# Kernel tuning notes

Measured on AMD Instinct MI355X. Metric: run time of the kernel, lower is better.

## Reference

```python
import jax, jax.numpy as jnp
import numpy as np

B, S, D = 2, 2048, 2048
H, DN, DR, DV = 16, 128, 64, 128   # heads, qk_nope, qk_rope, v_head
Q_LORA, KV_LORA = 1536, 512
DQ = DN + DR                        # qk_head_dim = 192
EPS = 1e-6


def setup_inputs() -> dict:
    key = jax.random.key(0)
    ks = jax.random.split(key, 8)
    s = 0.02  # weight init scale
    hidden_states = jax.random.normal(ks[0], (B, S, D), jnp.float32)
    # RoPE tables (non-interleaved HF style: cat(freqs, freqs)) per position
    inv_freq = 1.0 / (10000.0 ** (np.arange(0, DR, 2, dtype=np.float32) / DR))
    freqs = np.arange(S, dtype=np.float32)[:, None] * inv_freq[None, :]  # [S, DR/2]
    emb = np.concatenate([freqs, freqs], axis=-1)                        # [S, DR]
    cos = jnp.broadcast_to(jnp.asarray(np.cos(emb)), (B, S, DR))
    sin = jnp.broadcast_to(jnp.asarray(np.sin(emb)), (B, S, DR))
    return {
        'hidden_states': hidden_states,
        'cos': cos, 'sin': sin,
        'Wqa': jax.random.normal(ks[1], (D, Q_LORA), jnp.float32) * s,
        'qa_ln_w': jnp.ones((Q_LORA,), jnp.float32),
        'Wqb': jax.random.normal(ks[2], (Q_LORA, H * DQ), jnp.float32) * s,
        'Wkva': jax.random.normal(ks[3], (D, KV_LORA + DR), jnp.float32) * s,
        'kva_ln_w': jnp.ones((KV_LORA,), jnp.float32),
        'Wkvb': jax.random.normal(ks[4], (KV_LORA, H * (DN + DV)), jnp.float32) * s,
        'Wo': jax.random.normal(ks[5], (H * DV, D), jnp.float32) * s,
    }


def _rmsnorm(x, w):
    xf = x.astype(jnp.float32)
    var = jnp.mean(xf * xf, axis=-1, keepdims=True)
    return w * (xf * jax.lax.rsqrt(var + EPS)).astype(x.dtype)


def _rotate_half(x):
    h = x.shape[-1] // 2
    return jnp.concatenate([-x[..., h:], x[..., :h]], axis=-1)


def reference(hidden_states, cos, sin, Wqa, qa_ln_w, Wqb, Wkva, kva_ln_w, Wkvb, Wo):
    b, s, _ = hidden_states.shape
    scaling = DQ ** -0.5

    # Q path: down-proj -> RMSNorm -> up-proj -> [b, H, s, DQ]
    q = _rmsnorm(hidden_states @ Wqa, qa_ln_w) @ Wqb
    q = q.reshape(b, s, H, DQ).transpose(0, 2, 1, 3)
    q_pass, q_rot = q[..., :DN], q[..., DN:]

    # KV path: joint down-proj -> split latent / shared rope key
    ckv = hidden_states @ Wkva                       # [b, s, KV_LORA + DR]
    k_lat, k_rot = ckv[..., :KV_LORA], ckv[..., KV_LORA:]
    kv = _rmsnorm(k_lat, kva_ln_w) @ Wkvb            # [b, s, H*(DN+DV)]
    kv = kv.reshape(b, s, H, DN + DV).transpose(0, 2, 1, 3)
    k_pass, v = kv[..., :DN], kv[..., DN:]

    # decoupled RoPE on q_rot and the single shared k_rot head
    k_rot = k_rot[:, None, :, :]                     # [b, 1, s, DR]
    c, si = cos[:, None], sin[:, None]               # unsqueeze_dim=1
    q_rot = q_rot * c + _rotate_half(q_rot) * si
    k_rot = k_rot * c + _rotate_half(k_rot) * si
    k_rot = jnp.broadcast_to(k_rot, (b, H, s, DR))

    Q = jnp.concatenate([q_pass, q_rot], axis=-1)    # [b, H, s, DQ]
    K = jnp.concatenate([k_pass, k_rot], axis=-1)

    scores = jnp.einsum('bhqd,bhkd->bhqk', Q, K) * scaling
    neg = jnp.finfo(jnp.float32).min
    causal = jnp.where(jnp.tril(jnp.ones((s, s), bool)), 0.0, neg)
    scores = scores + causal
    w = jax.nn.softmax(scores.astype(jnp.float32), axis=-1).astype(Q.dtype)

    out = jnp.einsum('bhqk,bhkd->bhqd', w, v)
    out = out.transpose(0, 2, 1, 3).reshape(b, s, H * DV)
    return out @ Wo
```

## Files before the change

### kernel.cpp

```cpp
#include <hip/hip_runtime.h>
#include <math.h>

#define BB 2
#define SS 2048
#define DD 2048
#define HH 16
#define DN 128
#define DR 64
#define DV 128
#define QL 1536
#define KVL 512
#define DQ 192
#define CKVS 640
#define KVD 256
#define NCAT 2176
#define NCATP 2304
#define EPSF 1e-6f

typedef short bfrag __attribute__((ext_vector_type(8)));
typedef float facc  __attribute__((ext_vector_type(4)));

__device__ __forceinline__ ushort f2bf(float f) {
    union { float f; unsigned u; } v; v.f = f;
    unsigned r = v.u + 0x7fffu + ((v.u >> 16) & 1u);
    return (ushort)(r >> 16);
}
__device__ __forceinline__ float bf2f(ushort u) {
    union { unsigned u; float f; } v; v.u = ((unsigned)u) << 16;
    return v.f;
}
__device__ __forceinline__ float fexp2(float x) {
    float r; asm("v_exp_f32 %0, %1" : "=v"(r) : "v"(x)); return r;
}
__device__ __forceinline__ float wave_red_sum(float v) {
    #pragma unroll
    for (int o = 32; o > 0; o >>= 1) v += __shfl_down(v, o);
    return v;
}
__device__ __forceinline__ void gl2lds16(const ushort* g, ushort* l) {
    __builtin_amdgcn_global_load_lds(
        (const __attribute__((address_space(1))) void*)g,
        (__attribute__((address_space(3))) void*)l, 16, 0, 0);
}

__global__ __launch_bounds__(256) void castf2bf(const float* __restrict__ x,
                                                ushort* __restrict__ y) {
    const int i = blockIdx.x * 256 + threadIdx.x;
    const float4 v = ((const float4*)x)[i];
    ushort4 o;
    o.x = f2bf(v.x); o.y = f2bf(v.y); o.z = f2bf(v.z); o.w = f2bf(v.w);
    ((ushort4*)y)[i] = o;
}

struct WtBatch {
    const float* src[2];
    ushort* dst[2];
    int K[2];
    int N[2];
    int nx[2];
    int base[3];
};
__global__ __launch_bounds__(256) void wtrans_b(WtBatch d) {
    __shared__ float tile[32][33];
    int bid = blockIdx.x;
    int seg = (bid >= d.base[1]) ? 1 : 0;
    const int l = bid - d.base[seg];
    const int nx = d.nx[seg];
    const int bx = l % nx, by = l / nx;
    const float* W = d.src[seg];
    ushort* Wt = d.dst[seg];
    const int K = d.K[seg], N = d.N[seg];
    const int k0 = by * 32, n0 = bx * 32;
    const int t = threadIdx.x;
    const int tx = t & 31, ty = t >> 5;
    #pragma unroll
    for (int r = 0; r < 4; ++r) {
        const int n = n0 + tx;
        tile[ty + r * 8][tx] =
            (n < N) ? W[(size_t)(k0 + ty + r * 8) * N + n] : 0.f;
    }
    __syncthreads();
    #pragma unroll
    for (int r = 0; r < 4; ++r) {
        const int n = n0 + ty + r * 8;
        Wt[(size_t)n * K + k0 + tx] = f2bf(tile[tx][ty + r * 8]);
    }
}


__device__ __forceinline__ void stage_half(const ushort* __restrict__ G,
                                           int ldg, int grow0, int kcol0,
                                           ushort* Lr, int wave, int lane) {
    const int r0   = lane >> 3;
    const int slot = (lane & 7) ^ r0;
    const ushort* s0 = G + (size_t)(grow0 + wave * 16 + r0) * ldg + kcol0 + slot * 8;
    gl2lds16(s0,                    Lr + wave * 1024);
    gl2lds16(s0 + (size_t)8 * ldg,  Lr + wave * 1024 + 512);
}

#define PH_PRE  do { __builtin_amdgcn_sched_barrier(0);                      \
                     __builtin_amdgcn_s_barrier();                           \
                     asm volatile("s_waitcnt lgkmcnt(0)" ::: "memory");      \
                     __builtin_amdgcn_sched_barrier(0);                      \
                     __builtin_amdgcn_s_setprio(1); } while (0)
#define PH_POST do { __builtin_amdgcn_s_setprio(0);                          \
                     __builtin_amdgcn_sched_barrier(0);                      \
                     __builtin_amdgcn_s_barrier(); } while (0)

#define MFMA16(RB)                                                           \
    _Pragma("unroll")                                                        \
    for (int i = 0; i < 4; ++i)                                              \
        _Pragma("unroll")                                                    \
        for (int j = 0; j < 4; ++j)                                          \
            acc[(RB) + i][j] = __builtin_amdgcn_mfma_f32_16x16x32_bf16(      \
                a[i], b[j], acc[(RB) + i][j], 0, 0, 0);

#define GEMM256_CORE(A_, Bt_, K_, NBX_, LID_)                                 \
    const int t    = threadIdx.x;                                             \
    const int lane = t & 63;                                                  \
    const int wave = t >> 6;                                                  \
    const int wm   = wave >> 2;                                               \
    const int wn   = wave & 3;                                                \
    const int quad = lane >> 4;                                               \
    const int lrow = lane & 15;                                               \
    const int bx = (LID_) % (NBX_), by = (LID_) / (NBX_);                     \
    const int m0 = by * 256, n0 = bx * 256;                                   \
    const int s0x8  = (quad ^ (lrow & 7)) * 8;       \
    const int s1x8  = s0x8 ^ 32;                   \
    const int abase = lrow * 64;                                              \
    const int bbase = (wn & 1) * 4096 + lrow * 64;                            \
    facc acc[8][4];                                                           \
    _Pragma("unroll")                                                         \
    for (int i = 0; i < 8; ++i)                                               \
        _Pragma("unroll")                                                     \
        for (int j = 0; j < 4; ++j) acc[i][j] = (facc)(0.f);                  \
    const int nk = (K_) >> 6;                                                 \
    stage_half((A_),  (K_), m0,        0, L,         wave, lane);             \
    stage_half((A_),  (K_), m0 + 128,  0, L + 8192,  wave, lane);             \
    stage_half((Bt_), (K_), n0,        0, L + 16384, wave, lane);             \
    stage_half((Bt_), (K_), n0 + 128,  0, L + 24576, wave, lane);             \
    stage_half((Bt_), (K_), n0,       64, L + 49152, wave, lane);             \
    stage_half((Bt_), (K_), n0 + 128, 64, L + 57344, wave, lane);             \
    asm volatile("s_waitcnt vmcnt(4)" ::: "memory");                          \
    __builtin_amdgcn_s_barrier();                                             \
    for (int kt = 0; kt < nk; ++kt) {                                         \
        const int p = kt & 1;                                                 \
        ushort* LA = L + p * 32768 + wm * 8192;                               \
        ushort* LB = L + p * 32768 + 16384 + (wn >> 1) * 8192;                \
        ushort* Lq = L + (p ^ 1) * 32768;                                     \
        const int kn = (kt + 1) * 64;                                         \
        bfrag a[4], b[4];                                                     \
        _Pragma("unroll")                                                     \
        for (int i = 0; i < 4; ++i)                                           \
            a[i] = *(const bfrag*)(LA + i * 1024 + abase + s0x8);             \
        _Pragma("unroll")                                                     \
        for (int j = 0; j < 4; ++j)                                           \
            b[j] = *(const bfrag*)(LB + bbase + j * 1024 + s0x8);             \
        if (kt + 1 < nk) stage_half((A_), (K_), m0, kn, Lq, wave, lane);      \
        PH_PRE;                                                               \
        MFMA16(0)                                                             \
        PH_POST;                                                              \
        _Pragma("unroll")                                                     \
        for (int i = 0; i < 4; ++i)                                           \
            a[i] = *(const bfrag*)(LA + (4 + i) * 1024 + abase + s0x8);       \
        if (kt + 1 < nk)                                                      \
            stage_half((A_), (K_), m0 + 128, kn, Lq + 8192, wave, lane);      \
        PH_PRE;                                                               \
        MFMA16(4)                                                             \
        PH_POST;                                                              \
        _Pragma("unroll")                                                     \
        for (int i = 0; i < 4; ++i)                                           \
            a[i] = *(const bfrag*)(LA + i * 1024 + abase + s1x8);             \
        _Pragma("unroll")                                                     \
        for (int j = 0; j < 4; ++j)                                           \
            b[j] = *(const bfrag*)(LB + bbase + j * 1024 + s1x8);             \
        PH_PRE;                                                               \
        MFMA16(0)                                                             \
        PH_POST;                                                              \
        _Pragma("unroll")                                                     \
        for (int i = 0; i < 4; ++i)                                           \
            a[i] = *(const bfrag*)(LA + (4 + i) * 1024 + abase + s1x8);       \
        if (kt + 2 < nk) {                                                    \
            stage_half((Bt_), (K_), n0,       kn + 64,                        \
                       L + p * 32768 + 16384, wave, lane);                    \
            stage_half((Bt_), (K_), n0 + 128, kn + 64,                        \
                       L + p * 32768 + 24576, wave, lane);                    \
            asm volatile("s_waitcnt vmcnt(4)" ::: "memory");                  \
        } else {                                                              \
            asm volatile("s_waitcnt vmcnt(0)" ::: "memory");                  \
        }                                                                     \
        PH_PRE;                                                               \
        MFMA16(4)                                                             \
        PH_POST;                                                              \
    }

#define GEMMW_CORE(A_, Bt_, K_, NBX_, LID_)                                   \
    const int t    = threadIdx.x;                                             \
    const int lane = t & 63;                                                  \
    const int wave = t >> 6;                                                  \
    const int wm   = wave >> 1;                                     \
    const int wn   = wave & 1;                                      \
    const int quad = lane >> 4;                                               \
    const int lrow = lane & 15;                                               \
    const int bx = (LID_) % (NBX_), by = (LID_) / (NBX_);                     \
    const int m0 = by * 256, n0 = bx * 128;                                   \
    const int s0x8 = (quad ^ (lrow & 7)) * 8;                                 \
    const int s1x8 = s0x8 ^ 32;                                               \
    facc acc[4][4];                                                           \
    _Pragma("unroll")                                                         \
    for (int i = 0; i < 4; ++i)                                               \
        _Pragma("unroll")                                                     \
        for (int j = 0; j < 4; ++j) acc[i][j] = (facc)(0.f);                  \
    const int nk = (K_) >> 6;                                                 \
    stage_half((A_),  (K_), m0,        0, L,          wave, lane);            \
    stage_half((A_),  (K_), m0 + 128,  0, L + 8192,   wave, lane);            \
    stage_half((Bt_), (K_), n0,        0, L + 32768,  wave, lane);            \
    stage_half((Bt_), (K_), n0,       64, L + 40960,  wave, lane);            \
    asm volatile("s_waitcnt vmcnt(0)" ::: "memory");                          \
    __builtin_amdgcn_s_barrier();                                             \
    int bp = 0, bp2 = 2;                               \
    for (int kt = 0; kt < nk; ++kt) {                                         \
        const int p = kt & 1;                                                 \
        ushort* LA = L + p * 16384 + (wm >> 1) * 8192                         \
                       + ((wm & 1) * 64 + lrow) * 64;                         \
        ushort* LB = L + 32768 + bp * 8192 + (wn * 64 + lrow) * 64;           \
        const int kn = (kt + 1) * 64;                                         \
        bfrag a[4], b[4];                                                     \
        _Pragma("unroll")                                                     \
        for (int i = 0; i < 4; ++i) a[i] = *(const bfrag*)(LA + i * 1024 + s0x8); \
        _Pragma("unroll")                                                     \
        for (int j = 0; j < 4; ++j) b[j] = *(const bfrag*)(LB + j * 1024 + s0x8); \
        if (kt + 1 < nk) {                                                    \
            stage_half((A_), (K_), m0,       kn, L + (p ^ 1) * 16384,        wave, lane); \
            stage_half((A_), (K_), m0 + 128, kn, L + (p ^ 1) * 16384 + 8192, wave, lane); \
        }                                                                     \
        if (kt + 2 < nk)                                                      \
            stage_half((Bt_), (K_), n0, kn + 64, L + 32768 + bp2 * 8192, wave, lane); \
        PH_PRE;                                                               \
        MFMA16(0)                                                             \
        PH_POST;                                                              \
        _Pragma("unroll")                                                     \
        for (int i = 0; i < 4; ++i) a[i] = *(const bfrag*)(LA + i * 1024 + s1x8); \
        _Pragma("unroll")                                                     \
        for (int j = 0; j < 4; ++j) b[j] = *(const bfrag*)(LB + j * 1024 + s1x8); \
        if (kt + 2 < nk) { asm volatile("s_waitcnt vmcnt(2)" ::: "memory"); } \
        else             { asm volatile("s_waitcnt vmcnt(0)" ::: "memory"); } \
        PH_PRE;                                                               \
        MFMA16(0)                                                             \
        PH_POST;                                                              \
        bp  = (bp  == 2) ? 0 : bp  + 1;                                       \
        bp2 = (bp2 == 2) ? 0 : bp2 + 1;                                       \
    }

template <int K, int NBX, int NOUT>
__global__ __launch_bounds__(512, 2) void gemmW(const ushort* __restrict__ A,
                                                const ushort* __restrict__ Bt,
                                                float* __restrict__ C) {
    __shared__ ushort L[57344];
    int wg = (int)blockIdx.x;
    { const int cpx = (int)gridDim.x >> 3; wg = (wg & 7) * cpx + (wg >> 3); }
    GEMMW_CORE(A, Bt, K, NBX, wg)
    #pragma unroll
    for (int m = 0; m < 4; ++m) {
        const int row = m0 + wm * 64 + m * 16 + quad * 4;
        #pragma unroll
        for (int nf = 0; nf < 4; ++nf) {
            const int col = n0 + wn * 64 + nf * 16 + lrow;
            #pragma unroll
            for (int r = 0; r < 4; ++r)
                C[(size_t)(row + r) * NOUT + col] = acc[m][nf][r];
        }
    }
}

__global__ __launch_bounds__(512, 2) void gemmAW(
    const ushort* __restrict__ A,   const ushort* __restrict__ Bt,
    ushort* __restrict__ qa,        ushort* __restrict__ ckv,
    const float* __restrict__ Wqb,  ushort* __restrict__ Wqbt,
    const float* __restrict__ Wkvb, ushort* __restrict__ Wkvbt,
    const float* __restrict__ Wo,   ushort* __restrict__ Wot) {
    __shared__ ushort L[65536];
    const int bid = (int)blockIdx.x;
    if (bid < 144) {
        const int lid = (bid & 7) * 18 + (bid >> 3);
        GEMM256_CORE(A, Bt, DD, 9, lid)
        #pragma unroll
        for (int m = 0; m < 8; ++m) {
            const int row = m0 + wm * 128 + m * 16 + quad * 4;
            #pragma unroll
            for (int nf = 0; nf < 4; ++nf) {
                const int col = n0 + wn * 64 + nf * 16 + lrow;
                #pragma unroll
                for (int r = 0; r < 4; ++r) {
                    if (col < QL)
                        qa[(size_t)(row + r) * QL + col] = f2bf(acc[m][nf][r]);
                    else if (col < NCAT)
                        ckv[(size_t)(row + r) * CKVS + col - QL] = f2bf(acc[m][nf][r]);
                }
            }
        }
    } else {
        const int wid = bid - 144;
        const int t   = threadIdx.x;
        const int half = t >> 8;
        const int tl = t & 255;
        const int tx = tl & 31, ty = tl >> 5;
        float (*tile)[33] = (float(*)[33])((float*)L + half * 32 * 33);
        for (int it = 0; it < 48; ++it) {
            const int idx = (it * 112 + wid) * 2 + half;
            const float* W; ushort* Wt; int K, N, nx, l;
            if (idx < 4608)      { l = idx;        W = Wqb;  Wt = Wqbt;  K = QL;  N = HH * DQ;  nx = 96; }
            else if (idx < 6656) { l = idx - 4608; W = Wkvb; Wt = Wkvbt; K = KVL; N = HH * KVD; nx = 128; }
            else                 { l = idx - 6656; W = Wo;   Wt = Wot;   K = DD;  N = DD;       nx = 64; }
            const int bx2 = l % nx, by2 = l / nx;
            const int k0 = by2 * 32, n0w = bx2 * 32;
            #pragma unroll
            for (int r = 0; r < 4; ++r)
                tile[ty + r * 8][tx] = W[(size_t)(k0 + ty + r * 8) * N + n0w + tx];
            __syncthreads();
            #pragma unroll
            for (int r = 0; r < 4; ++r)
                Wt[(size_t)(n0w + ty + r * 8) * K + k0 + tx] = f2bf(tile[tx][ty + r * 8]);
            __syncthreads();
        }
    }
}

__global__ __launch_bounds__(512, 2) void gemmQKV(
    const ushort* __restrict__ qa,  const ushort* __restrict__ Wqbt,
    ushort* __restrict__ Qbuf,
    const ushort* __restrict__ kvn, const ushort* __restrict__ Wkvbt,
    ushort* __restrict__ kvb) {
    __shared__ ushort L[65536];
    const int bid = (int)blockIdx.x;
    if (bid < 192) {
        const int lid = (bid & 7) * 24 + (bid >> 3);
        GEMM256_CORE(qa, Wqbt, QL, 12, lid)
        const float scaling = 0.10411754831f;
        #pragma unroll
        for (int m = 0; m < 8; ++m) {
            const int row = m0 + wm * 128 + m * 16 + quad * 4;
            #pragma unroll
            for (int nf = 0; nf < 4; ++nf) {
                const int col = n0 + wn * 64 + nf * 16 + lrow;
                const int h = col / DQ, d = col - h * DQ;
                #pragma unroll
                for (int r = 0; r < 4; ++r) {
                    const int tok = row + r;
                    const int b = tok >> 11, s2 = tok & (SS - 1);
                    Qbuf[((size_t)(b * HH + h) * SS + s2) * DQ + d] =
                        f2bf(acc[m][nf][r] * scaling);
                }
            }
        }
    } else {
        const int b2 = bid - 192;
        const int lid = (b2 & 7) * 32 + (b2 >> 3);
        GEMM256_CORE(kvn, Wkvbt, KVL, 16, lid)
        #pragma unroll
        for (int m = 0; m < 8; ++m) {
            const int row = m0 + wm * 128 + m * 16 + quad * 4;
            #pragma unroll
            for (int nf = 0; nf < 4; ++nf) {
                const int col = n0 + wn * 64 + nf * 16 + lrow;
                #pragma unroll
                for (int r = 0; r < 4; ++r)
                    kvb[(size_t)(row + r) * (HH * KVD) + col] = f2bf(acc[m][nf][r]);
            }
        }
    }
}

__global__ __launch_bounds__(256) void rmsnorm2(ushort* __restrict__ qa,
                                                const float* __restrict__ qaw,
                                                const ushort* __restrict__ ckv,
                                                const float* __restrict__ kvw,
                                                ushort* __restrict__ kvn,
                                                ushort* __restrict__ krb,
                                                const float* __restrict__ cosb,
                                                const float* __restrict__ sinb) {
    __shared__ float red[4];
    const int t = threadIdx.x;
    const int lane = t & 63, wid = t >> 6;
    const int bid = (int)blockIdx.x;
    if (bid < BB * SS) {
        ushort* xr = qa + (size_t)bid * QL;
        float ss = 0.f;
        for (int i = t; i < QL; i += 256) { float v = bf2f(xr[i]); ss += v * v; }
        ss = wave_red_sum(ss);
        if (lane == 0) red[wid] = ss;
        __syncthreads();
        const float tot = red[0] + red[1] + red[2] + red[3];
        const float sc = rsqrtf(tot / (float)QL + EPSF);
        for (int i = t; i < QL; i += 256) xr[i] = f2bf(qaw[i] * bf2f(xr[i]) * sc);
    } else {
        const int row = bid - BB * SS;
        const ushort* xr = ckv + (size_t)row * CKVS;
        ushort* yr = kvn + (size_t)row * KVL;
        if (t < 64) {
            const int p = t;
            const ushort* kin = xr + KVL;
            const float c  = cosb[(size_t)row * DR + p];
            const float sn = sinb[(size_t)row * DR + p];
            const float self = bf2f(kin[p]);
            const float partner = bf2f(kin[p < 32 ? p + 32 : p - 32]);
            const float v = (p < 32) ? (self * c - partner * sn)
                                     : (self * c + partner * sn);
            krb[(size_t)row * DR + p] = f2bf(v);
        }
        float ss = 0.f;
        for (int i = t; i < KVL; i += 256) { float v = bf2f(xr[i]); ss += v * v; }
        ss = wave_red_sum(ss);
        if (lane == 0) red[wid] = ss;
        __syncthreads();
        const float tot = red[0] + red[1] + red[2] + red[3];
        const float sc = rsqrtf(tot / (float)KVL + EPSF);
        for (int i = t; i < KVL; i += 256) yr[i] = f2bf(kvw[i] * bf2f(xr[i]) * sc);
    }
}

__global__ __launch_bounds__(256) void ropevprep(ushort* __restrict__ Qbuf,
                                                 const float* __restrict__ cosb,
                                                 const float* __restrict__ sinb,
                                                 const ushort* __restrict__ kvb,
                                                 ushort* __restrict__ Vtb) {
    __shared__ ushort tile[32][33];
    const int bid = (int)blockIdx.x;
    const int t = threadIdx.x;
    if (bid < BB * SS) {
        const int tok = bid;
        const int b = tok >> 11, s = tok & (SS - 1);
        const int p = t & 31, hh = t >> 5;
        const float c0 = cosb[(size_t)tok * DR + p];
        const float s0 = sinb[(size_t)tok * DR + p];
        const float c1 = cosb[(size_t)tok * DR + p + 32];
        const float s1 = sinb[(size_t)tok * DR + p + 32];
        #pragma unroll
        for (int it = 0; it < 2; ++it) {
            const int h = hh + it * 8;
            ushort* base = Qbuf + ((size_t)(b * HH + h) * SS + s) * DQ + DN;
            const float x0 = bf2f(base[p]), x1 = bf2f(base[p + 32]);
            base[p]      = f2bf(x0 * c0 - x1 * s0);
            base[p + 32] = f2bf(x1 * c1 + x0 * s1);
        }
    } else {
        const int v = bid - BB * SS;
        const int kp0 = (v & 63) * 32;
        const int dv0 = ((v >> 6) & 3) * 32;
        const int bh  = v >> 8;
        const int b = bh / HH, h = bh - b * HH;
        const int tx = t & 31, ty = t >> 5;
        #pragma unroll
        for (int r = 0; r < 4; ++r)
            tile[ty + r * 8][tx] =
                kvb[(size_t)(b * SS + kp0 + ty + r * 8) * (HH * KVD) + h * KVD + DN + dv0 + tx];
        __syncthreads();
        #pragma unroll
        for (int r = 0; r < 4; ++r)
            Vtb[((size_t)bh * DV + dv0 + ty + r * 8) * SS + kp0 + tx] = tile[tx][ty + r * 8];
    }
}

__global__ __launch_bounds__(256, 2) void fattn_mfma(
    const ushort* __restrict__ Qb,
    const ushort* __restrict__ kvb,
    const ushort* __restrict__ krb,
    const ushort* __restrict__ Vt,
    ushort* __restrict__ o)
{
    const int h  = blockIdx.y;
    const int b  = blockIdx.z;
    const int qt = b ? (15 - (int)blockIdx.x) : (int)blockIdx.x;
    const int bh = b * HH + h;
    const int q0 = qt * 128;
    const int t    = threadIdx.x;
    const int lane = t & 63;
    const int wave = t >> 6;
    const int quad = lane >> 4;
    const int n    = lane & 15;
    const int wstrip = wave * 16;

    __shared__ ushort Ksu[6 * 64 * 32];
    __shared__ ushort Vtu[2 * 128 * 32];
    __shared__ ushort Psu[2 * 128 * 40];

    const ushort* vbase = Vt + (size_t)bh * DV * SS;

    bfrag aQ[2][6];
    #pragma unroll
    for (int sp = 0; sp < 2; ++sp) {
        const ushort* qrow = Qb + ((size_t)bh * SS + q0 + sp * 64 + wstrip + n) * DQ;
        #pragma unroll
        for (int kb = 0; kb < 6; ++kb)
            aQ[sp][kb] = *(const bfrag*)(qrow + kb * 32 + quad * 8);
    }

    facc oacc[2][8];
    float lp[2][4];
    #pragma unroll
    for (int sp = 0; sp < 2; ++sp) {
        #pragma unroll
        for (int jd = 0; jd < 8; ++jd) oacc[sp][jd] = (facc)(0.f);
        #pragma unroll
        for (int r = 0; r < 4; ++r) lp[sp][r] = 0.f;
    }

    #pragma unroll
    for (int i = 0; i < 6; ++i) {
        const int g = wave + 4 * i;
        const int kb = g >> 2;
        const int rem = (g & 3) * 64 + lane;
        const int row = rem >> 2, sub = rem & 3;
        const int tok = b * SS + row;
        const ushort* src = (kb < 4)
            ? kvb + (size_t)tok * (HH * KVD) + h * KVD + kb * 32 + sub * 8
            : krb + (size_t)tok * DR + (kb - 4) * 32 + sub * 8;
        gl2lds16(src, Ksu + g * 512);
    }
    #pragma unroll
    for (int i = 0; i < 4; ++i) {
        const int g = wave + 4 * i;
        const int kb2 = g >> 3;
        const int rem = (g & 7) * 64 + lane;
        const int dv = rem >> 2, sub = rem & 3;
        gl2lds16(vbase + (size_t)dv * SS + kb2 * 32 + sub * 8, Vtu + g * 512);
    }
    __syncthreads();

    const int nkt = 2 * qt + 2;
    for (int kt = 0; kt < nkt; ++kt) {
        const int k0 = kt * 64;
        const int kk = (kt + 1 < nkt) ? (k0 + 64) : (SS - 64);

        bfrag kreg[6], vreg[4];
        #pragma unroll
        for (int i = 0; i < 6; ++i) {
            const int g = wave + 4 * i;
            const int kb = g >> 2;
            const int rem = (g & 3) * 64 + lane;
            const int row = rem >> 2, sub = rem & 3;
            const int tok = b * SS + kk + row;
            const ushort* src = (kb < 4)
                ? kvb + (size_t)tok * (HH * KVD) + h * KVD + kb * 32 + sub * 8
                : krb + (size_t)tok * DR + (kb - 4) * 32 + sub * 8;
            kreg[i] = *(const bfrag*)src;
        }
        #pragma unroll
        for (int i = 0; i < 4; ++i) {
            const int g = wave + 4 * i;
            const int kb2 = g >> 3;
            const int rem = (g & 7) * 64 + lane;
            const int dv = rem >> 2, sub = rem & 3;
            vreg[i] = *(const bfrag*)(vbase + (size_t)dv * SS + kk + kb2 * 32 + sub * 8);
        }
        __builtin_amdgcn_sched_barrier(0);

        facc s[2][4];
        #pragma unroll
        for (int sp = 0; sp < 2; ++sp)
            #pragma unroll
            for (int j = 0; j < 4; ++j) s[sp][j] = (facc)(0.f);
        #pragma unroll
        for (int kb = 0; kb < 6; ++kb) {
            #pragma unroll
            for (int j = 0; j < 4; ++j) {
                const bfrag bk =
                    *(const bfrag*)&Ksu[kb * 2048 + (j * 16 + n) * 32 + quad * 8];
                s[0][j] = __builtin_amdgcn_mfma_f32_16x16x32_bf16(aQ[0][kb], bk, s[0][j], 0, 0, 0);
                s[1][j] = __builtin_amdgcn_mfma_f32_16x16x32_bf16(aQ[1][kb], bk, s[1][j], 0, 0, 0);
            }
        }

        const bool fullt = (k0 + 64 <= q0);
        if (fullt) {
            #pragma unroll
            for (int sp = 0; sp < 2; ++sp) {
                #pragma unroll
                for (int j = 0; j < 4; ++j) {
                    #pragma unroll
                    for (int r = 0; r < 4; ++r) {
                        const float p = fexp2(s[sp][j][r]);
                        lp[sp][r] += p;
                        Psu[(j >> 1) * 5120 + (sp * 64 + wstrip + quad * 4 + r) * 40
                            + (j & 1) * 16 + n] = f2bf(p);
                    }
                }
            }
        } else {
            #pragma unroll
            for (int sp = 0; sp < 2; ++sp) {
                const int rowg0 = q0 + sp * 64 + wstrip + quad * 4;
                #pragma unroll
                for (int j = 0; j < 4; ++j) {
                    const int kpos = k0 + j * 16 + n;
                    #pragma unroll
                    for (int r = 0; r < 4; ++r) {
                        const float p = (kpos <= rowg0 + r) ? fexp2(s[sp][j][r]) : 0.f;
                        lp[sp][r] += p;
                        Psu[(j >> 1) * 5120 + (sp * 64 + wstrip + quad * 4 + r) * 40
                            + (j & 1) * 16 + n] = f2bf(p);
                    }
                }
            }
        }

        #pragma unroll
        for (int kb2 = 0; kb2 < 2; ++kb2) {
            const bfrag aP0 = *(const bfrag*)&Psu[kb2 * 5120 + (wstrip + n) * 40 + quad * 8];
            const bfrag aP1 = *(const bfrag*)&Psu[kb2 * 5120 + (64 + wstrip + n) * 40 + quad * 8];
            #pragma unroll
            for (int jd = 0; jd < 8; ++jd) {
                const bfrag bV = *(const bfrag*)&Vtu[kb2 * 4096 + (jd * 16 + n) * 32 + quad * 8];
                oacc[0][jd] = __builtin_amdgcn_mfma_f32_16x16x32_bf16(aP0, bV, oacc[0][jd], 0, 0, 0);
                oacc[1][jd] = __builtin_amdgcn_mfma_f32_16x16x32_bf16(aP1, bV, oacc[1][jd], 0, 0, 0);
            }
        }

        __syncthreads();
        #pragma unroll
        for (int i = 0; i < 6; ++i)
            *(bfrag*)(Ksu + (wave + 4 * i) * 512 + lane * 8) = kreg[i];
        #pragma unroll
        for (int i = 0; i < 4; ++i)
            *(bfrag*)(Vtu + (wave + 4 * i) * 512 + lane * 8) = vreg[i];
        __syncthreads();
    }

    #pragma unroll
    for (int sp = 0; sp < 2; ++sp) {
        #pragma unroll
        for (int r = 0; r < 4; ++r) {
            float v = lp[sp][r];
            #pragma unroll
            for (int msk = 1; msk < 16; msk <<= 1) v += __shfl_xor(v, msk);
            const float inv = 1.f / v;
            ushort* op = o + (size_t)(b * SS + q0 + sp * 64 + wstrip + quad * 4 + r)
                             * (HH * DV) + h * DV;
            #pragma unroll
            for (int jd = 0; jd < 8; ++jd)
                op[jd * 16 + n] = f2bf(oacc[sp][jd][r] * inv);
        }
    }
}

extern "C" void kernel_launch(void* const* d_in, const int* in_sizes, int n_in,
                              void* d_out, int out_size, void* d_ws, size_t ws_size,
                              hipStream_t stream) {
    const float* hs    = (const float*)d_in[0];
    const float* cosb  = (const float*)d_in[1];
    const float* sinb  = (const float*)d_in[2];
    const float* Wqa   = (const float*)d_in[3];
    const float* qa_w  = (const float*)d_in[4];
    const float* Wqb   = (const float*)d_in[5];
    const float* Wkva  = (const float*)d_in[6];
    const float* kva_w = (const float*)d_in[7];
    const float* Wkvb  = (const float*)d_in[8];
    const float* Wo    = (const float*)d_in[9];
    float* out = (float*)d_out;

    const int T = BB * SS;

    char* w = (char*)d_ws;
    auto alloc = [&](size_t bytes) {
        void* r = (void*)w;
        w += (bytes + 255) & ~(size_t)255;
        return r;
    };
    ushort* hs_bf  = (ushort*)alloc((size_t)T * DD * 2);
    ushort* Wcat   = (ushort*)alloc((size_t)NCATP * DD * 2);
    ushort* Wqbt   = (ushort*)alloc((size_t)(HH * DQ) * QL * 2);
    ushort* Wkvbt  = (ushort*)alloc((size_t)(HH * KVD) * KVL * 2);
    ushort* Wot    = (ushort*)alloc((size_t)DD * DD * 2);
    ushort* qa_bf  = (ushort*)alloc((size_t)T * QL * 2);
    ushort* Qbuf   = (ushort*)alloc((size_t)T * HH * DQ * 2);
    ushort* ckv_bf = (ushort*)alloc((size_t)T * CKVS * 2);
    ushort* kvn_bf = (ushort*)alloc((size_t)T * KVL * 2);
    ushort* kv_bf  = (ushort*)alloc((size_t)T * HH * KVD * 2);
    ushort* krb    = (ushort*)alloc((size_t)T * DR * 2);
    ushort* Vtb    = Wcat;
    ushort* ao_bf  = hs_bf;

    castf2bf<<<(T * DD / 4) / 256, 256, 0, stream>>>(hs, hs_bf);
    WtBatch wb;
    wb.src[0] = Wqa;  wb.dst[0] = Wcat;                   wb.K[0] = DD; wb.N[0] = QL;       wb.nx[0] = 48;
    wb.src[1] = Wkva; wb.dst[1] = Wcat + (size_t)QL * DD; wb.K[1] = DD; wb.N[1] = KVL + DR; wb.nx[1] = 20;
    wb.base[0] = 0;
    wb.base[1] = wb.nx[0] * (DD / 32);
    wb.base[2] = wb.base[1] + wb.nx[1] * (DD / 32);
    wtrans_b<<<wb.base[2], 256, 0, stream>>>(wb);

    gemmAW<<<dim3(256), 512, 0, stream>>>(hs_bf, Wcat, qa_bf, ckv_bf,
                                          Wqb, Wqbt, Wkvb, Wkvbt, Wo, Wot);
    rmsnorm2<<<2 * T, 256, 0, stream>>>(qa_bf, qa_w, ckv_bf, kva_w, kvn_bf,
                                        krb, cosb, sinb);
    gemmQKV<<<dim3(448), 512, 0, stream>>>(qa_bf, Wqbt, Qbuf,
                                           kvn_bf, Wkvbt, kv_bf);
    ropevprep<<<T + 8192, 256, 0, stream>>>(Qbuf, cosb, sinb, kv_bf, Vtb);
    fattn_mfma<<<dim3(16, HH, BB), 256, 0, stream>>>(Qbuf, kv_bf, krb, Vtb, ao_bf);
    gemmW<DD, 16, DD><<<dim3(256), 512, 0, stream>>>(ao_bf, Wot, out);
}
```

Measured before the change: 403.0 us.

## Split attention strips across 8 waves and use 256x256 tiles for output GEMM

The flash-attention kernel now runs with 512 threads per block, so each wave handles one 16-row query strip instead of two. This halves per-wave registers and raises the occupancy bound to 4. The output projection drops the 256x128-tile gemmW and uses the existing 256x256 GEMM256 core with 128 blocks, which gives more reuse per tile. The risk is fewer blocks for the output GEMM, plus fewer MFMAs per LDS load and more LDS contention in attention.

```diff
diff --git a/kernel.cpp b/kernel.cpp
--- a/kernel.cpp
+++ b/kernel.cpp
@@ -194,81 +194,22 @@
         PH_POST;                                                              \
     }
 
-#define GEMMW_CORE(A_, Bt_, K_, NBX_, LID_)                                   \
-    const int t    = threadIdx.x;                                             \
-    const int lane = t & 63;                                                  \
-    const int wave = t >> 6;                                                  \
-    const int wm   = wave >> 1;                                     \
-    const int wn   = wave & 1;                                      \
-    const int quad = lane >> 4;                                               \
-    const int lrow = lane & 15;                                               \
-    const int bx = (LID_) % (NBX_), by = (LID_) / (NBX_);                     \
-    const int m0 = by * 256, n0 = bx * 128;                                   \
-    const int s0x8 = (quad ^ (lrow & 7)) * 8;                                 \
-    const int s1x8 = s0x8 ^ 32;                                               \
-    facc acc[4][4];                                                           \
-    _Pragma("unroll")                                                         \
-    for (int i = 0; i < 4; ++i)                                               \
-        _Pragma("unroll")                                                     \
-        for (int j = 0; j < 4; ++j) acc[i][j] = (facc)(0.f);                  \
-    const int nk = (K_) >> 6;                                                 \
-    stage_half((A_),  (K_), m0,        0, L,          wave, lane);            \
-    stage_half((A_),  (K_), m0 + 128,  0, L + 8192,   wave, lane);            \
-    stage_half((Bt_), (K_), n0,        0, L + 32768,  wave, lane);            \
-    stage_half((Bt_), (K_), n0,       64, L + 40960,  wave, lane);            \
-    asm volatile("s_waitcnt vmcnt(0)" ::: "memory");                          \
-    __builtin_amdgcn_s_barrier();                                             \
-    int bp = 0, bp2 = 2;                               \
-    for (int kt = 0; kt < nk; ++kt) {                                         \
-        const int p = kt & 1;                                                 \
-        ushort* LA = L + p * 16384 + (wm >> 1) * 8192                         \
-                       + ((wm & 1) * 64 + lrow) * 64;                         \
-        ushort* LB = L + 32768 + bp * 8192 + (wn * 64 + lrow) * 64;           \
-        const int kn = (kt + 1) * 64;                                         \
-        bfrag a[4], b[4];                                                     \
-        _Pragma("unroll")                                                     \
-        for (int i = 0; i < 4; ++i) a[i] = *(const bfrag*)(LA + i * 1024 + s0x8); \
-        _Pragma("unroll")                                                     \
-        for (int j = 0; j < 4; ++j) b[j] = *(const bfrag*)(LB + j * 1024 + s0x8); \
-        if (kt + 1 < nk) {                                                    \
-            stage_half((A_), (K_), m0,       kn, L + (p ^ 1) * 16384,        wave, lane); \
-            stage_half((A_), (K_), m0 + 128, kn, L + (p ^ 1) * 16384 + 8192, wave, lane); \
-        }                                                                     \
-        if (kt + 2 < nk)                                                      \
-            stage_half((Bt_), (K_), n0, kn + 64, L + 32768 + bp2 * 8192, wave, lane); \
-        PH_PRE;                                                               \
-        MFMA16(0)                                                             \
-        PH_POST;                                                              \
-        _Pragma("unroll")                                                     \
-        for (int i = 0; i < 4; ++i) a[i] = *(const bfrag*)(LA + i * 1024 + s1x8); \
-        _Pragma("unroll")                                                     \
-        for (int j = 0; j < 4; ++j) b[j] = *(const bfrag*)(LB + j * 1024 + s1x8); \
-        if (kt + 2 < nk) { asm volatile("s_waitcnt vmcnt(2)" ::: "memory"); } \
-        else             { asm volatile("s_waitcnt vmcnt(0)" ::: "memory"); } \
-        PH_PRE;                                                               \
-        MFMA16(0)                                                             \
-        PH_POST;                                                              \
-        bp  = (bp  == 2) ? 0 : bp  + 1;                                       \
-        bp2 = (bp2 == 2) ? 0 : bp2 + 1;                                       \
-    }
-
-template <int K, int NBX, int NOUT>
-__global__ __launch_bounds__(512, 2) void gemmW(const ushort* __restrict__ A,
+__global__ __launch_bounds__(512, 2) void gemmO(const ushort* __restrict__ A,
                                                 const ushort* __restrict__ Bt,
                                                 float* __restrict__ C) {
-    __shared__ ushort L[57344];
-    int wg = (int)blockIdx.x;
-    { const int cpx = (int)gridDim.x >> 3; wg = (wg & 7) * cpx + (wg >> 3); }
-    GEMMW_CORE(A, Bt, K, NBX, wg)
-    #pragma unroll
-    for (int m = 0; m < 4; ++m) {
-        const int row = m0 + wm * 64 + m * 16 + quad * 4;
+    __shared__ ushort L[65536];
+    const int bid = (int)blockIdx.x;
+    const int lid = (bid & 7) * 16 + (bid >> 3);
+    GEMM256_CORE(A, Bt, DD, 8, lid)
+    #pragma unroll
+    for (int m = 0; m < 8; ++m) {
+        const int row = m0 + wm * 128 + m * 16 + quad * 4;
         #pragma unroll
         for (int nf = 0; nf < 4; ++nf) {
             const int col = n0 + wn * 64 + nf * 16 + lrow;
             #pragma unroll
             for (int r = 0; r < 4; ++r)
-                C[(size_t)(row + r) * NOUT + col] = acc[m][nf][r];
+                C[(size_t)(row + r) * DD + col] = acc[m][nf][r];
         }
     }
 }
@@ -461,7 +402,7 @@
     }
 }
 
-__global__ __launch_bounds__(256, 2) void fattn_mfma(
+__global__ __launch_bounds__(512, 4) void fattn_mfma(
     const ushort* __restrict__ Qb,
     const ushort* __restrict__ kvb,
     const ushort* __restrict__ krb,
@@ -486,28 +427,24 @@
 
     const ushort* vbase = Vt + (size_t)bh * DV * SS;
 
-    bfrag aQ[2][6];
-    #pragma unroll
-    for (int sp = 0; sp < 2; ++sp) {
-        const ushort* qrow = Qb + ((size_t)bh * SS + q0 + sp * 64 + wstrip + n) * DQ;
+    bfrag aQ[6];
+    {
+        const ushort* qrow = Qb + ((size_t)bh * SS + q0 + wstrip + n) * DQ;
         #pragma unroll
         for (int kb = 0; kb < 6; ++kb)
-            aQ[sp][kb] = *(const bfrag*)(qrow + kb * 32 + quad * 8);
-    }
-
-    facc oacc[2][8];
-    float lp[2][4];
-    #pragma unroll
-    for (int sp = 0; sp < 2; ++sp) {
-        #pragma unroll
-        for (int jd = 0; jd < 8; ++jd) oacc[sp][jd] = (facc)(0.f);
-        #pragma unroll
-        for (int r = 0; r < 4; ++r) lp[sp][r] = 0.f;
-    }
-
-    #pragma unroll
-    for (int i = 0; i < 6; ++i) {
-        const int g = wave + 4 * i;
+            aQ[kb] = *(const bfrag*)(qrow + kb * 32 + quad * 8);
+    }
+
+    facc oacc[8];
+    float lp[4];
+    #pragma unroll
+    for (int jd = 0; jd < 8; ++jd) oacc[jd] = (facc)(0.f);
+    #pragma unroll
+    for (int r = 0; r < 4; ++r) lp[r] = 0.f;
+
+    #pragma unroll
+    for (int i = 0; i < 3; ++i) {
+        const int g = wave + 8 * i;
         const int kb = g >> 2;
         const int rem = (g & 3) * 64 + lane;
         const int row = rem >> 2, sub = rem & 3;
@@ -518,8 +455,8 @@
         gl2lds16(src, Ksu + g * 512);
     }
     #pragma unroll
-    for (int i = 0; i < 4; ++i) {
-        const int g = wave + 4 * i;
+    for (int i = 0; i < 2; ++i) {
+        const int g = wave + 8 * i;
         const int kb2 = g >> 3;
         const int rem = (g & 7) * 64 + lane;
         const int dv = rem >> 2, sub = rem & 3;
@@ -532,10 +469,10 @@
         const int k0 = kt * 64;
         const int kk = (kt + 1 < nkt) ? (k0 + 64) : (SS - 64);
 
-        bfrag kreg[6], vreg[4];
-        #pragma unroll
-        for (int i = 0; i < 6; ++i) {
-            const int g = wave + 4 * i;
+        bfrag kreg[3], vreg[2];
+        #pragma unroll
+        for (int i = 0; i < 3; ++i) {
+            const int g = wave + 8 * i;
             const int kb = g >> 2;
             const int rem = (g & 3) * 64 + lane;
             const int row = rem >> 2, sub = rem & 3;
@@ -546,8 +483,8 @@
             kreg[i] = *(const bfrag*)src;
         }
         #pragma unroll
-        for (int i = 0; i < 4; ++i) {
-            const int g = wave + 4 * i;
+        for (int i = 0; i < 2; ++i) {
+            const int g = wave + 8 * i;
             const int kb2 = g >> 3;
             const int rem = (g & 7) * 64 + lane;
             const int dv = rem >> 2, sub = rem & 3;
@@ -555,91 +492,77 @@
         }
         __builtin_amdgcn_sched_barrier(0);
 
-        facc s[2][4];
-        #pragma unroll
-        for (int sp = 0; sp < 2; ++sp)
-            #pragma unroll
-            for (int j = 0; j < 4; ++j) s[sp][j] = (facc)(0.f);
+        facc s[4];
+        #pragma unroll
+        for (int j = 0; j < 4; ++j) s[j] = (facc)(0.f);
         #pragma unroll
         for (int kb = 0; kb < 6; ++kb) {
             #pragma unroll
             for (int j = 0; j < 4; ++j) {
                 const bfrag bk =
                     *(const bfrag*)&Ksu[kb * 2048 + (j * 16 + n) * 32 + quad * 8];
-                s[0][j] = __builtin_amdgcn_mfma_f32_16x16x32_bf16(aQ[0][kb], bk, s[0][j], 0, 0, 0);
-                s[1][j] = __builtin_amdgcn_mfma_f32_16x16x32_bf16(aQ[1][kb], bk, s[1][j], 0, 0, 0);
+                s[j] = __builtin_amdgcn_mfma_f32_16x16x32_bf16(aQ[kb], bk, s[j], 0, 0, 0);
             }
         }
 
         const bool fullt = (k0 + 64 <= q0);
         if (fullt) {
             #pragma unroll
-            for (int sp = 0; sp < 2; ++sp) {
+            for (int j = 0; j < 4; ++j) {
                 #pragma unroll
-                for (int j = 0; j < 4; ++j) {
-                    #pragma unroll
-                    for (int r = 0; r < 4; ++r) {
-                        const float p = fexp2(s[sp][j][r]);
-                        lp[sp][r] += p;
-                        Psu[(j >> 1) * 5120 + (sp * 64 + wstrip + quad * 4 + r) * 40
-                            + (j & 1) * 16 + n] = f2bf(p);
-                    }
+                for (int r = 0; r < 4; ++r) {
+                    const float p = fexp2(s[j][r]);
+                    lp[r] += p;
+                    Psu[(j >> 1) * 5120 + (wstrip + quad * 4 + r) * 40
+                        + (j & 1) * 16 + n] = f2bf(p);
                 }
             }
         } else {
-            #pragma unroll
-            for (int sp = 0; sp < 2; ++sp) {
-                const int rowg0 = q0 + sp * 64 + wstrip + quad * 4;
+            const int rowg0 = q0 + wstrip + quad * 4;
+            #pragma unroll
+            for (int j = 0; j < 4; ++j) {
+                const int kpos = k0 + j * 16 + n;
                 #pragma unroll
-                for (int j = 0; j < 4; ++j) {
-                    const int kpos = k0 + j * 16 + n;
-                    #pragma unroll
-                    for (int r = 0; r < 4; ++r) {
-                        const float p = (kpos <= rowg0 + r) ? fexp2(s[sp][j][r]) : 0.f;
-                        lp[sp][r] += p;
-                        Psu[(j >> 1) * 5120 + (sp * 64 + wstrip + quad * 4 + r) * 40
-                            + (j & 1) * 16 + n] = f2bf(p);
-                    }
+                for (int r = 0; r < 4; ++r) {
+                    const float p = (kpos <= rowg0 + r) ? fexp2(s[j][r]) : 0.f;
+                    lp[r] += p;
+                    Psu[(j >> 1) * 5120 + (wstrip + quad * 4 + r) * 40
+                        + (j & 1) * 16 + n] = f2bf(p);
                 }
             }
         }
 
         #pragma unroll
         for (int kb2 = 0; kb2 < 2; ++kb2) {
-            const bfrag aP0 = *(const bfrag*)&Psu[kb2 * 5120 + (wstrip + n) * 40 + quad * 8];
-            const bfrag aP1 = *(const bfrag*)&Psu[kb2 * 5120 + (64 + wstrip + n) * 40 + quad * 8];
+            const bfrag aP = *(const bfrag*)&Psu[kb2 * 5120 + (wstrip + n) * 40 + quad * 8];
             #pragma unroll
             for (int jd = 0; jd < 8; ++jd) {
                 const bfrag bV = *(const bfrag*)&Vtu[kb2 * 4096 + (jd * 16 + n) * 32 + quad * 8];
-                oacc[0][jd] = __builtin_amdgcn_mfma_f32_16x16x32_bf16(aP0, bV, oacc[0][jd], 0, 0, 0);
-                oacc[1][jd] = __builtin_amdgcn_mfma_f32_16x16x32_bf16(aP1, bV, oacc[1][jd], 0, 0, 0);
+                oacc[jd] = __builtin_amdgcn_mfma_f32_16x16x32_bf16(aP, bV, oacc[jd], 0, 0, 0);
             }
         }
 
         __syncthreads();
         #pragma unroll
-        for (int i = 0; i < 6; ++i)
-            *(bfrag*)(Ksu + (wave + 4 * i) * 512 + lane * 8) = kreg[i];
-        #pragma unroll
-        for (int i = 0; i < 4; ++i)
-            *(bfrag*)(Vtu + (wave + 4 * i) * 512 + lane * 8) = vreg[i];
+        for (int i = 0; i < 3; ++i)
+            *(bfrag*)(Ksu + (wave + 8 * i) * 512 + lane * 8) = kreg[i];
+        #pragma unroll
+        for (int i = 0; i < 2; ++i)
+            *(bfrag*)(Vtu + (wave + 8 * i) * 512 + lane * 8) = vreg[i];
         __syncthreads();
     }
 
     #pragma unroll
-    for (int sp = 0; sp < 2; ++sp) {
-        #pragma unroll
-        for (int r = 0; r < 4; ++r) {
-            float v = lp[sp][r];
-            #pragma unroll
-            for (int msk = 1; msk < 16; msk <<= 1) v += __shfl_xor(v, msk);
-            const float inv = 1.f / v;
-            ushort* op = o + (size_t)(b * SS + q0 + sp * 64 + wstrip + quad * 4 + r)
-                             * (HH * DV) + h * DV;
-            #pragma unroll
-            for (int jd = 0; jd < 8; ++jd)
-                op[jd * 16 + n] = f2bf(oacc[sp][jd][r] * inv);
-        }
+    for (int r = 0; r < 4; ++r) {
+        float v = lp[r];
+        #pragma unroll
+        for (int msk = 1; msk < 16; msk <<= 1) v += __shfl_xor(v, msk);
+        const float inv = 1.f / v;
+        ushort* op = o + (size_t)(b * SS + q0 + wstrip + quad * 4 + r)
+                         * (HH * DV) + h * DV;
+        #pragma unroll
+        for (int jd = 0; jd < 8; ++jd)
+            op[jd * 16 + n] = f2bf(oacc[jd][r] * inv);
     }
 }
 
@@ -696,6 +619,6 @@
     gemmQKV<<<dim3(448), 512, 0, stream>>>(qa_bf, Wqbt, Qbuf,
                                            kvn_bf, Wkvbt, kv_bf);
     ropevprep<<<T + 8192, 256, 0, stream>>>(Qbuf, cosb, sinb, kv_bf, Vtb);
-    fattn_mfma<<<dim3(16, HH, BB), 256, 0, stream>>>(Qbuf, kv_bf, krb, Vtb, ao_bf);
-    gemmW<DD, 16, DD><<<dim3(256), 512, 0, stream>>>(ao_bf, Wot, out);
-}
+    fattn_mfma<<<dim3(16, HH, BB), 512, 0, stream>>>(Qbuf, kv_bf, krb, Vtb, ao_bf);
+    gemmO<<<dim3(128), 512, 0, stream>>>(ao_bf, Wot, out);
+}
```

Result: slower. 451.9 us (+12.1%).
